# Performance work log

Measured on AMD Instinct MI355X. Metric: run time of the kernel, lower is better.

Reference implementation:

```python
import jax, jax.numpy as jnp
import numpy as np

B, T, C, H = 2, 2048, 1024, 16
HS = C // H  # head size = 64


def setup_inputs() -> dict:
    key = jax.random.key(0)
    k1, k2, k3 = jax.random.split(key, 3)
    X = jax.random.normal(k1, (B, T, C), dtype=jnp.float32)
    W_qkv = jax.random.normal(k2, (C, 3 * C), dtype=jnp.float32) * (C ** -0.5)
    W_proj = jax.random.normal(k3, (C, C), dtype=jnp.float32) * (C ** -0.5)
    return {"X": X, "W_qkv": W_qkv, "W_proj": W_proj}


def reference(X, W_qkv, W_proj):
    b, t, c = X.shape
    h, hs = H, c // H
    qkv = X @ W_qkv                      # [b,t,3c]
    k_, q_, v_ = jnp.split(qkv, 3, axis=2)  # module order: K, Q, V
    K = k_.reshape(b, t, h, hs).transpose(0, 2, 1, 3)  # [b,h,t,hs]
    Q = q_.reshape(b, t, h, hs).transpose(0, 2, 1, 3)
    V = v_.reshape(b, t, h, hs).transpose(0, 2, 1, 3)
    # NOTE: original scales by full embed dim c**-0.5 (not head_size)
    scores = jnp.einsum('bhqd,bhkd->bhqk', Q, K) * (c ** -0.5)
    causal = jnp.tril(jnp.ones((t, t), dtype=bool))
    scores = jnp.where(causal, scores, -jnp.inf)
    W = jax.nn.softmax(scores, axis=-1)  # dropout is identity in eval mode
    out = jnp.einsum('bhqk,bhkd->bhqd', W, V)  # [b,h,t,hs]
    out = out.transpose(0, 2, 1, 3).reshape(b, t, c)
    return out @ W_proj
```

## Files before the change

### kernel.cpp

```cpp
#include <hip/hip_runtime.h>

#define TB 2
#define TT 2048
#define TC 1024
#define TH 16
#define THS 64

typedef short bf16x8 __attribute__((ext_vector_type(8)));
typedef float f32x4 __attribute__((ext_vector_type(4)));

#define QSCALE 0.0450842200278f

__device__ inline unsigned short f2b(float f) {
    unsigned u = __builtin_bit_cast(unsigned, f);
    unsigned r = (u + 0x7fffu + ((u >> 16) & 1u)) >> 16;
    return (unsigned short)r;
}
__device__ inline float b2f(unsigned short h) {
    unsigned u = ((unsigned)h) << 16;
    return __builtin_bit_cast(float, u);
}

__device__ inline void gl_lds16(const unsigned short* g, unsigned short* l) {
    __builtin_amdgcn_global_load_lds(
        (const __attribute__((address_space(1))) unsigned int*)(g),
        (__attribute__((address_space(3))) unsigned int*)(l), 16, 0, 0);
}

__device__ inline float dpp_sum16(float x) {
    int t;
    t = __builtin_amdgcn_update_dpp(0, __builtin_bit_cast(int, x), 0x128, 0xf, 0xf, true);
    x += __builtin_bit_cast(float, t);
    t = __builtin_amdgcn_update_dpp(0, __builtin_bit_cast(int, x), 0x124, 0xf, 0xf, true);
    x += __builtin_bit_cast(float, t);
    t = __builtin_amdgcn_update_dpp(0, __builtin_bit_cast(int, x), 0x122, 0xf, 0xf, true);
    x += __builtin_bit_cast(float, t);
    t = __builtin_amdgcn_update_dpp(0, __builtin_bit_cast(int, x), 0x121, 0xf, 0xf, true);
    x += __builtin_bit_cast(float, t);
    return x;
}

__global__ void cvt_bf16_k(const float* __restrict__ in, unsigned short* __restrict__ out) {
    const int i = blockIdx.x * blockDim.x + threadIdx.x;
    const float4* p = (const float4*)in + (size_t)i * 2;
    const float4 a = p[0], b = p[1];
    bf16x8 v;
    v[0] = (short)f2b(a.x); v[1] = (short)f2b(a.y);
    v[2] = (short)f2b(a.z); v[3] = (short)f2b(a.w);
    v[4] = (short)f2b(b.x); v[5] = (short)f2b(b.y);
    v[6] = (short)f2b(b.z); v[7] = (short)f2b(b.w);
    *(bf16x8*)(out + (size_t)i * 8) = v;
}

__global__ void transpose_cvt_k(const float* __restrict__ in,
                                unsigned short* __restrict__ out, int R, int Cc) {
    __shared__ float tile[32][33];
    const int tx = threadIdx.x, ty = threadIdx.y;
    const int r0 = blockIdx.y * 32, c0 = blockIdx.x * 32;
#pragma unroll
    for (int i = 0; i < 4; i++)
        tile[ty + i * 8][tx] = in[(size_t)(r0 + ty + i * 8) * Cc + c0 + tx];
    __syncthreads();
#pragma unroll
    for (int i = 0; i < 4; i++)
        out[(size_t)(c0 + ty + i * 8) * R + r0 + tx] = f2b(tile[tx][ty + i * 8]);
}

__global__ void vt_k(const unsigned short* __restrict__ Vb,
                     unsigned short* __restrict__ Vt) {
    __shared__ unsigned short tile[32][33];
    const int tx = threadIdx.x, ty = threadIdx.y;
    const int d0 = blockIdx.x * 32, t0 = blockIdx.y * 32, bh = blockIdx.z;
    const unsigned short* src = Vb + (size_t)bh * TT * THS;
    unsigned short* dst = Vt + (size_t)bh * THS * TT;
#pragma unroll
    for (int i = 0; i < 4; i++)
        tile[ty + i * 8][tx] = src[(size_t)(t0 + ty + i * 8) * THS + d0 + tx];
    __syncthreads();
#pragma unroll
    for (int i = 0; i < 4; i++)
        dst[(size_t)(d0 + ty + i * 8) * TT + t0 + tx] = tile[tx][ty + i * 8];
}

__global__ __launch_bounds__(256) void gemm_qkv(
    const unsigned short* __restrict__ A, const unsigned short* __restrict__ Bt, int K,
    unsigned short* __restrict__ outK, unsigned short* __restrict__ outQ,
    unsigned short* __restrict__ outV) {
    __shared__ __align__(16) unsigned short As[128 * 32];
    __shared__ __align__(16) unsigned short Bs[128 * 32];

    const int tid = threadIdx.x;
    const int wave = tid >> 6, lane = tid & 63;
    const int quad = lane >> 4, l16 = lane & 15;
    const int wm = (wave >> 1) * 64, wn = (wave & 1) * 64;
    const int m0 = blockIdx.y * 128, n0 = blockIdx.x * 128;

    const f32x4 vzero = {0.f, 0.f, 0.f, 0.f};
    f32x4 acc[4][4];
#pragma unroll
    for (int i = 0; i < 4; i++)
#pragma unroll
        for (int j = 0; j < 4; j++) acc[i][j] = vzero;

    const int nk = K >> 5;
    for (int kt = 0; kt < nk; ++kt) {
        const int k0 = kt * 32;
        __syncthreads();
#pragma unroll
        for (int it = 0; it < 2; ++it) {
            const int chunk = tid + it * 256;
            const int r = chunk >> 2, col = (chunk & 3) * 8;
            gl_lds16(A + (size_t)(m0 + r) * K + k0 + col, &As[chunk * 8]);
            gl_lds16(Bt + (size_t)(n0 + r) * K + k0 + col, &Bs[chunk * 8]);
        }
        __syncthreads();
        bf16x8 af[4], bfr[4];
#pragma unroll
        for (int f = 0; f < 4; ++f) {
            af[f] = *(const bf16x8*)(&As[(wm + f * 16 + l16) * 32 + quad * 8]);
            bfr[f] = *(const bf16x8*)(&Bs[(wn + f * 16 + l16) * 32 + quad * 8]);
        }
#pragma unroll
        for (int fm = 0; fm < 4; ++fm)
#pragma unroll
            for (int fn = 0; fn < 4; ++fn)
                acc[fm][fn] = __builtin_amdgcn_mfma_f32_16x16x32_bf16(
                    af[fm], bfr[fn], acc[fm][fn], 0, 0, 0);
    }

#pragma unroll
    for (int fm = 0; fm < 4; ++fm) {
#pragma unroll
        for (int fn = 0; fn < 4; ++fn) {
#pragma unroll
            for (int r = 0; r < 4; ++r) {
                const int row = m0 + wm + fm * 16 + quad * 4 + r;
                const int col = n0 + wn + fn * 16 + l16;
                const float val = acc[fm][fn][r];
                const int b = row >> 11, t = row & (TT - 1);
                const int chunkc = col >> 10, cc = col & (TC - 1);
                const int hh = cc >> 6, d = cc & 63;
                const size_t idx = (size_t)((b * TH + hh) * TT + t) * THS + d;
                if (chunkc == 0)
                    outK[idx] = f2b(val);
                else if (chunkc == 1)
                    outQ[idx] = f2b(val * QSCALE);
                else
                    outV[idx] = f2b(val);
            }
        }
    }
}

__global__ __launch_bounds__(256) void gemm_proj(
    const unsigned short* __restrict__ A, const unsigned short* __restrict__ Bt,
    int M, int N, int K, float* __restrict__ outF) {
    __shared__ __align__(16) unsigned short As[128 * 32];
    __shared__ __align__(16) unsigned short Bs[64 * 32];

    const int tid = threadIdx.x;
    const int wave = tid >> 6, lane = tid & 63;
    const int quad = lane >> 4, l16 = lane & 15;
    const int wm = wave * 32;
    const int m0 = blockIdx.y * 128, n0 = blockIdx.x * 64;

    const f32x4 vzero = {0.f, 0.f, 0.f, 0.f};
    f32x4 acc[2][4];
#pragma unroll
    for (int i = 0; i < 2; i++)
#pragma unroll
        for (int j = 0; j < 4; j++) acc[i][j] = vzero;

    const int nk = K >> 5;
    for (int kt = 0; kt < nk; ++kt) {
        const int k0 = kt * 32;
        __syncthreads();
#pragma unroll
        for (int it = 0; it < 2; ++it) {
            const int chunk = tid + it * 256;
            const int r = chunk >> 2, col = (chunk & 3) * 8;
            gl_lds16(A + (size_t)(m0 + r) * K + k0 + col, &As[chunk * 8]);
        }
        {
            const int r = tid >> 2, col = (tid & 3) * 8;
            gl_lds16(Bt + (size_t)(n0 + r) * K + k0 + col, &Bs[tid * 8]);
        }
        __syncthreads();
        bf16x8 af[2], bfr[4];
#pragma unroll
        for (int f = 0; f < 2; ++f)
            af[f] = *(const bf16x8*)(&As[(wm + f * 16 + l16) * 32 + quad * 8]);
#pragma unroll
        for (int f = 0; f < 4; ++f)
            bfr[f] = *(const bf16x8*)(&Bs[(f * 16 + l16) * 32 + quad * 8]);
#pragma unroll
        for (int fm = 0; fm < 2; ++fm)
#pragma unroll
            for (int fn = 0; fn < 4; ++fn)
                acc[fm][fn] = __builtin_amdgcn_mfma_f32_16x16x32_bf16(
                    af[fm], bfr[fn], acc[fm][fn], 0, 0, 0);
    }

#pragma unroll
    for (int fm = 0; fm < 2; ++fm)
#pragma unroll
        for (int fn = 0; fn < 4; ++fn)
#pragma unroll
            for (int r = 0; r < 4; ++r) {
                const int row = m0 + wm + fm * 16 + quad * 4 + r;
                const int col = n0 + fn * 16 + l16;
                outF[(size_t)row * N + col] = acc[fm][fn][r];
            }
}

__global__ __launch_bounds__(256, 3) void attn_k(
    const unsigned short* __restrict__ Qb, const unsigned short* __restrict__ Kb,
    const unsigned short* __restrict__ Vt, unsigned short* __restrict__ AO) {
    __shared__ __align__(16) unsigned short U[4][2304];
    __shared__ float lS[4][32];

    const int tid = threadIdx.x;
    const int w = tid >> 6, lane = tid & 63;
    const int quad = lane >> 4, l16 = lane & 15;
    const int bh = blockIdx.x;
    const int qtt = 63 - blockIdx.y;
    const int q0 = qtt * 32;
    const unsigned short* Qh = Qb + (size_t)bh * TT * THS;
    const unsigned short* Kh = Kb + (size_t)bh * TT * THS;
    const unsigned short* Vh = Vt + (size_t)bh * THS * TT;

    bf16x8 aQ[2][2];
#pragma unroll
    for (int rt = 0; rt < 2; ++rt)
#pragma unroll
        for (int ks = 0; ks < 2; ++ks)
            aQ[rt][ks] = *(const bf16x8*)(
                Qh + (size_t)(q0 + rt * 16 + l16) * THS + ks * 32 + quad * 8);

    const float NEGINF = -__builtin_inff();
    const f32x4 vzero = {0.f, 0.f, 0.f, 0.f};
    f32x4 o[2][4];
    float lp[2][4];
#pragma unroll
    for (int rt = 0; rt < 2; ++rt)
#pragma unroll
        for (int i = 0; i < 4; i++) { o[rt][i] = vzero; lp[rt][i] = 0.f; }

    const int nkt = (qtt >> 1) + 1;
    for (int kt = w; kt < nkt; kt += 4) {
        const int t0 = kt * 64;
        bf16x8 bK[8], bV[8];
#pragma unroll
        for (int nt = 0; nt < 4; ++nt)
#pragma unroll
            for (int ks = 0; ks < 2; ++ks) {
                bK[nt * 2 + ks] = *(const bf16x8*)(
                    Kh + (size_t)(t0 + nt * 16 + l16) * THS + ks * 32 + quad * 8);
                bV[nt * 2 + ks] = *(const bf16x8*)(
                    Vh + (size_t)(nt * 16 + l16) * TT + t0 + ks * 32 + quad * 8);
            }
        const bool needmask = (kt == nkt - 1);
#pragma unroll
        for (int rt = 0; rt < 2; ++rt) {
            f32x4 s[4];
#pragma unroll
            for (int nt = 0; nt < 4; ++nt) s[nt] = vzero;
#pragma unroll
            for (int ks = 0; ks < 2; ++ks)
#pragma unroll
                for (int nt = 0; nt < 4; ++nt)
                    s[nt] = __builtin_amdgcn_mfma_f32_16x16x32_bf16(
                        aQ[rt][ks], bK[nt * 2 + ks], s[nt], 0, 0, 0);
            unsigned short* Pw = &U[w][0] + rt * 1152;
#pragma unroll
            for (int r = 0; r < 4; ++r) {
                const int row = q0 + rt * 16 + quad * 4 + r;
                float v0 = s[0][r], v1 = s[1][r], v2 = s[2][r], v3 = s[3][r];
                if (needmask) {
                    if (t0 + l16 > row) v0 = NEGINF;
                    if (t0 + 16 + l16 > row) v1 = NEGINF;
                    if (t0 + 32 + l16 > row) v2 = NEGINF;
                    if (t0 + 48 + l16 > row) v3 = NEGINF;
                }
                const float p0 = __builtin_amdgcn_exp2f(v0);
                const float p1 = __builtin_amdgcn_exp2f(v1);
                const float p2 = __builtin_amdgcn_exp2f(v2);
                const float p3 = __builtin_amdgcn_exp2f(v3);
                lp[rt][r] += (p0 + p1) + (p2 + p3);
                const int pr = (quad * 4 + r) * 72;
                Pw[pr + l16] = f2b(p0);
                Pw[pr + 16 + l16] = f2b(p1);
                Pw[pr + 32 + l16] = f2b(p2);
                Pw[pr + 48 + l16] = f2b(p3);
            }
        }
        asm volatile("s_waitcnt lgkmcnt(0)" ::: "memory");
        bf16x8 aP[2][2];
#pragma unroll
        for (int rt = 0; rt < 2; ++rt) {
            const unsigned short* Pw = &U[w][0] + rt * 1152;
            aP[rt][0] = *(const bf16x8*)(Pw + l16 * 72 + quad * 8);
            aP[rt][1] = *(const bf16x8*)(Pw + l16 * 72 + 32 + quad * 8);
        }
#pragma unroll
        for (int rt = 0; rt < 2; ++rt)
#pragma unroll
            for (int ks = 0; ks < 2; ++ks)
#pragma unroll
                for (int nt = 0; nt < 4; ++nt)
                    o[rt][nt] = __builtin_amdgcn_mfma_f32_16x16x32_bf16(
                        aP[rt][ks], bV[nt * 2 + ks], o[rt][nt], 0, 0, 0);
    }

#pragma unroll
    for (int rt = 0; rt < 2; ++rt)
#pragma unroll
        for (int r = 0; r < 4; ++r) {
            const float lsum = dpp_sum16(lp[rt][r]);
            const int row = rt * 16 + quad * 4 + r;
            if (l16 == 0) lS[w][row] = lsum;
#pragma unroll
            for (int nt = 0; nt < 4; ++nt)
                U[w][row * 66 + nt * 16 + l16] = f2b(o[rt][nt][r]);
        }
    __syncthreads();

    const int b = bh >> 4, h = bh & 15;
    const int col = w * 16 + l16;
#pragma unroll
    for (int rr = 0; rr < 8; ++rr) {
        const int row = quad * 8 + rr;
        const float L = (lS[0][row] + lS[1][row]) + (lS[2][row] + lS[3][row]);
        const float O = (b2f(U[0][row * 66 + col]) + b2f(U[1][row * 66 + col])) +
                        (b2f(U[2][row * 66 + col]) + b2f(U[3][row * 66 + col]));
        const int t = q0 + row;
        AO[((size_t)(b * TT + t)) * TC + h * 64 + col] = f2b(O * __builtin_amdgcn_rcpf(L));
    }
}

extern "C" void kernel_launch(void* const* d_in, const int* in_sizes, int n_in,
                              void* d_out, int out_size, void* d_ws, size_t ws_size,
                              hipStream_t stream) {
    const float* X = (const float*)d_in[0];
    const float* Wqkv = (const float*)d_in[1];
    const float* Wproj = (const float*)d_in[2];
    float* out = (float*)d_out;

    unsigned short* ws = (unsigned short*)d_ws;
    unsigned short* Xb = ws;
    unsigned short* Wq_t = Xb + 4096 * 1024;
    unsigned short* Wp_t = Wq_t + 3072 * 1024;
    unsigned short* Qb = Wp_t + 1024 * 1024;
    unsigned short* Kb = Qb + TB * TH * TT * THS;
    unsigned short* Vb = Kb + TB * TH * TT * THS;
    unsigned short* Vt = Vb + TB * TH * TT * THS;
    unsigned short* AO = Vt + TB * TH * TT * THS;

    cvt_bf16_k<<<dim3((4096 * 1024) / (8 * 256)), 256, 0, stream>>>(X, Xb);
    transpose_cvt_k<<<dim3(3072 / 32, 1024 / 32), dim3(32, 8), 0, stream>>>(Wqkv, Wq_t, 1024, 3072);
    transpose_cvt_k<<<dim3(1024 / 32, 1024 / 32), dim3(32, 8), 0, stream>>>(Wproj, Wp_t, 1024, 1024);
    gemm_qkv<<<dim3(3072 / 128, 4096 / 128), 256, 0, stream>>>(Xb, Wq_t, 1024, Kb, Qb, Vb);
    vt_k<<<dim3(THS / 32, TT / 32, TB * TH), dim3(32, 8), 0, stream>>>(Vb, Vt);
    attn_k<<<dim3(32, 64), 256, 0, stream>>>(Qb, Kb, Vt, AO);
    gemm_proj<<<dim3(1024 / 64, 4096 / 128), 256, 0, stream>>>(
        AO, Wp_t, 4096, 1024, 1024, out);
}
```

Baseline: 213.5 us.

## Merge prep kernels, widen V transpose, hoist QKV epilogue branch, prefetch K tiles

Merges the X conversion and the two weight transposes into one launch, cutting two kernel launches. The V transpose now works on 64x64 tiles with one-dimensional blocks. The QKV GEMM epilogue picks its output pointer and scale once per block rather than branching per element. The attention loop double-buffers K fragments so the next tile's K loads are issued before the current tile's compute, at the cost of more registers.

Result: slower. 268.8 us (+25.9%).

```diff
diff --git a/kernel.cpp b/kernel.cpp
--- a/kernel.cpp
+++ b/kernel.cpp
@@ -40,23 +40,37 @@
     return x;
 }
 
-__global__ void cvt_bf16_k(const float* __restrict__ in, unsigned short* __restrict__ out) {
-    const int i = blockIdx.x * blockDim.x + threadIdx.x;
-    const float4* p = (const float4*)in + (size_t)i * 2;
-    const float4 a = p[0], b = p[1];
-    bf16x8 v;
-    v[0] = (short)f2b(a.x); v[1] = (short)f2b(a.y);
-    v[2] = (short)f2b(a.z); v[3] = (short)f2b(a.w);
-    v[4] = (short)f2b(b.x); v[5] = (short)f2b(b.y);
-    v[6] = (short)f2b(b.z); v[7] = (short)f2b(b.w);
-    *(bf16x8*)(out + (size_t)i * 8) = v;
-}
-
-__global__ void transpose_cvt_k(const float* __restrict__ in,
-                                unsigned short* __restrict__ out, int R, int Cc) {
+__global__ void prep_k(const float* __restrict__ X, const float* __restrict__ Wqkv,
+                       const float* __restrict__ Wproj, unsigned short* __restrict__ Xb,
+                       unsigned short* __restrict__ Wq_t, unsigned short* __restrict__ Wp_t) {
     __shared__ float tile[32][33];
-    const int tx = threadIdx.x, ty = threadIdx.y;
-    const int r0 = blockIdx.y * 32, c0 = blockIdx.x * 32;
+    const int tid = threadIdx.x;
+    const int bid = blockIdx.x;
+    if (bid < 2048) {
+        const int i = bid * 256 + tid;
+        const float4* p = (const float4*)X + (size_t)i * 2;
+        const float4 a = p[0], b = p[1];
+        bf16x8 v;
+        v[0] = (short)f2b(a.x); v[1] = (short)f2b(a.y);
+        v[2] = (short)f2b(a.z); v[3] = (short)f2b(a.w);
+        v[4] = (short)f2b(b.x); v[5] = (short)f2b(b.y);
+        v[6] = (short)f2b(b.z); v[7] = (short)f2b(b.w);
+        *(bf16x8*)(Xb + (size_t)i * 8) = v;
+        return;
+    }
+    const float* in;
+    unsigned short* out;
+    int R, Cc, c0, r0;
+    if (bid < 5120) {
+        const int b = bid - 2048;
+        in = Wqkv; out = Wq_t; R = 1024; Cc = 3072;
+        c0 = (b % 96) * 32; r0 = (b / 96) * 32;
+    } else {
+        const int b = bid - 5120;
+        in = Wproj; out = Wp_t; R = 1024; Cc = 1024;
+        c0 = (b & 31) * 32; r0 = (b >> 5) * 32;
+    }
+    const int tx = tid & 31, ty = tid >> 5;
 #pragma unroll
     for (int i = 0; i < 4; i++)
         tile[ty + i * 8][tx] = in[(size_t)(r0 + ty + i * 8) * Cc + c0 + tx];
@@ -68,18 +82,19 @@
 
 __global__ void vt_k(const unsigned short* __restrict__ Vb,
                      unsigned short* __restrict__ Vt) {
-    __shared__ unsigned short tile[32][33];
-    const int tx = threadIdx.x, ty = threadIdx.y;
-    const int d0 = blockIdx.x * 32, t0 = blockIdx.y * 32, bh = blockIdx.z;
+    __shared__ unsigned short tile[64][68];
+    const int tid = threadIdx.x;
+    const int tx = tid & 63, ty = tid >> 6;
+    const int t0 = blockIdx.x * 64, bh = blockIdx.y;
     const unsigned short* src = Vb + (size_t)bh * TT * THS;
     unsigned short* dst = Vt + (size_t)bh * THS * TT;
 #pragma unroll
-    for (int i = 0; i < 4; i++)
-        tile[ty + i * 8][tx] = src[(size_t)(t0 + ty + i * 8) * THS + d0 + tx];
+    for (int i = 0; i < 16; i++)
+        tile[ty + i * 4][tx] = src[(size_t)(t0 + ty + i * 4) * THS + tx];
     __syncthreads();
 #pragma unroll
-    for (int i = 0; i < 4; i++)
-        dst[(size_t)(d0 + ty + i * 8) * TT + t0 + tx] = tile[tx][ty + i * 8];
+    for (int i = 0; i < 16; i++)
+        dst[(size_t)(ty + i * 4) * TT + t0 + tx] = tile[tx][ty + i * 4];
 }
 
 __global__ __launch_bounds__(256) void gemm_qkv(
@@ -128,6 +143,9 @@
                     af[fm], bfr[fn], acc[fm][fn], 0, 0, 0);
     }
 
+    const int chunkc = n0 >> 10;
+    unsigned short* outp = (chunkc == 0) ? outK : ((chunkc == 1) ? outQ : outV);
+    const float mul = (chunkc == 1) ? QSCALE : 1.0f;
 #pragma unroll
     for (int fm = 0; fm < 4; ++fm) {
 #pragma unroll
@@ -136,17 +154,10 @@
             for (int r = 0; r < 4; ++r) {
                 const int row = m0 + wm + fm * 16 + quad * 4 + r;
                 const int col = n0 + wn + fn * 16 + l16;
-                const float val = acc[fm][fn][r];
                 const int b = row >> 11, t = row & (TT - 1);
-                const int chunkc = col >> 10, cc = col & (TC - 1);
+                const int cc = col & (TC - 1);
                 const int hh = cc >> 6, d = cc & 63;
-                const size_t idx = (size_t)((b * TH + hh) * TT + t) * THS + d;
-                if (chunkc == 0)
-                    outK[idx] = f2b(val);
-                else if (chunkc == 1)
-                    outQ[idx] = f2b(val * QSCALE);
-                else
-                    outV[idx] = f2b(val);
+                outp[(size_t)((b * TH + hh) * TT + t) * THS + d] = f2b(acc[fm][fn][r] * mul);
             }
         }
     }
@@ -247,18 +258,26 @@
         for (int i = 0; i < 4; i++) { o[rt][i] = vzero; lp[rt][i] = 0.f; }
 
     const int nkt = (qtt >> 1) + 1;
-    for (int kt = w; kt < nkt; kt += 4) {
+
+    auto loadK = [&](bf16x8(&bK)[4][2], int t0) {
+#pragma unroll
+        for (int nt = 0; nt < 4; ++nt)
+#pragma unroll
+            for (int ks = 0; ks < 2; ++ks)
+                bK[nt][ks] = *(const bf16x8*)(
+                    Kh + (size_t)(t0 + nt * 16 + l16) * THS + ks * 32 + quad * 8);
+    };
+
+    auto step = [&](bf16x8(&bKc)[4][2], bf16x8(&bKn)[4][2], int kt, int ktn) {
         const int t0 = kt * 64;
-        bf16x8 bK[8], bV[8];
+        bf16x8 bV[4][2];
 #pragma unroll
         for (int nt = 0; nt < 4; ++nt)
 #pragma unroll
-            for (int ks = 0; ks < 2; ++ks) {
-                bK[nt * 2 + ks] = *(const bf16x8*)(
-                    Kh + (size_t)(t0 + nt * 16 + l16) * THS + ks * 32 + quad * 8);
-                bV[nt * 2 + ks] = *(const bf16x8*)(
+            for (int ks = 0; ks < 2; ++ks)
+                bV[nt][ks] = *(const bf16x8*)(
                     Vh + (size_t)(nt * 16 + l16) * TT + t0 + ks * 32 + quad * 8);
-            }
+        if (ktn < nkt) loadK(bKn, ktn * 64);
         const bool needmask = (kt == nkt - 1);
 #pragma unroll
         for (int rt = 0; rt < 2; ++rt) {
@@ -270,7 +289,7 @@
 #pragma unroll
                 for (int nt = 0; nt < 4; ++nt)
                     s[nt] = __builtin_amdgcn_mfma_f32_16x16x32_bf16(
-                        aQ[rt][ks], bK[nt * 2 + ks], s[nt], 0, 0, 0);
+                        aQ[rt][ks], bKc[nt][ks], s[nt], 0, 0, 0);
             unsigned short* Pw = &U[w][0] + rt * 1152;
 #pragma unroll
             for (int r = 0; r < 4; ++r) {
@@ -309,7 +328,21 @@
 #pragma unroll
                 for (int nt = 0; nt < 4; ++nt)
                     o[rt][nt] = __builtin_amdgcn_mfma_f32_16x16x32_bf16(
-                        aP[rt][ks], bV[nt * 2 + ks], o[rt][nt], 0, 0, 0);
+                        aP[rt][ks], bV[nt][ks], o[rt][nt], 0, 0, 0);
+    };
+
+    bf16x8 K0[4][2], K1[4][2];
+    int kt = w;
+    if (kt < nkt) {
+        loadK(K0, kt * 64);
+        while (true) {
+            step(K0, K1, kt, kt + 4);
+            kt += 4;
+            if (kt >= nkt) break;
+            step(K1, K0, kt, kt + 4);
+            kt += 4;
+            if (kt >= nkt) break;
+        }
     }
 
 #pragma unroll
@@ -356,11 +389,9 @@
     unsigned short* Vt = Vb + TB * TH * TT * THS;
     unsigned short* AO = Vt + TB * TH * TT * THS;
 
-    cvt_bf16_k<<<dim3((4096 * 1024) / (8 * 256)), 256, 0, stream>>>(X, Xb);
-    transpose_cvt_k<<<dim3(3072 / 32, 1024 / 32), dim3(32, 8), 0, stream>>>(Wqkv, Wq_t, 1024, 3072);
-    transpose_cvt_k<<<dim3(1024 / 32, 1024 / 32), dim3(32, 8), 0, stream>>>(Wproj, Wp_t, 1024, 1024);
+    prep_k<<<dim3(6144), 256, 0, stream>>>(X, Wqkv, Wproj, Xb, Wq_t, Wp_t);
     gemm_qkv<<<dim3(3072 / 128, 4096 / 128), 256, 0, stream>>>(Xb, Wq_t, 1024, Kb, Qb, Vb);
-    vt_k<<<dim3(THS / 32, TT / 32, TB * TH), dim3(32, 8), 0, stream>>>(Vb, Vt);
+    vt_k<<<dim3(TT / 64, TB * TH), 256, 0, stream>>>(Vb, Vt);
     attn_k<<<dim3(32, 64), 256, 0, stream>>>(Qb, Kb, Vt, AO);
     gemm_proj<<<dim3(1024 / 64, 4096 / 128), 256, 0, stream>>>(
         AO, Wp_t, 4096, 1024, 1024, out);
```
